# Performance work log

Measured on AMD Instinct MI355X. Metric: run time of the kernel, lower is better.

Reference implementation:

```python
import jax, jax.numpy as jnp
import numpy as np

B, T, D, U, P, E = 32, 10, 10, 50, 50, 256
EPS_ATTN = 1e-8
EPS_LN = 1e-5


def _layer_norm(x, w, b):
    mu = jnp.mean(x, axis=-1, keepdims=True)
    var = jnp.mean((x - mu) ** 2, axis=-1, keepdims=True)
    return (x - mu) / jnp.sqrt(var + EPS_LN) * w + b


def setup_inputs() -> dict:
    key = jax.random.key(0)
    ks = jax.random.split(key, 8)
    xavier = float(np.sqrt(2.0 / (E + E)))
    return {
        "Q": jax.random.normal(ks[0], (B, T, U, E), dtype=jnp.float32),
        "K": jax.random.normal(ks[1], (B, D, P, E), dtype=jnp.float32),
        "V": jax.random.normal(ks[2], (B, D, P, E), dtype=jnp.float32),
        "attention_mask": jnp.zeros((B, T, D, U, P), dtype=jnp.float32),
        "W1": jax.random.normal(ks[3], (E, E), dtype=jnp.float32) * xavier,
        "b1": jnp.zeros((E,), dtype=jnp.float32),
        "W2": jax.random.normal(ks[4], (E, E), dtype=jnp.float32) * xavier,
        "b2": jnp.zeros((E,), dtype=jnp.float32),
        "ln1_w": jnp.ones((E,), dtype=jnp.float32),
        "ln1_b": jnp.zeros((E,), dtype=jnp.float32),
        "ln2_w": jnp.ones((E,), dtype=jnp.float32),
        "ln2_b": jnp.zeros((E,), dtype=jnp.float32),
    }


def reference(Q, K, V, attention_mask, W1, b1, W2, b2, ln1_w, ln1_b, ln2_w, ln2_b):
    # dk = max(1.0, emb_dim); scale = sqrt(dk) + eps
    scale = jnp.sqrt(jnp.asarray(float(max(1.0, Q.shape[-1])), dtype=Q.dtype)) + EPS_ATTN
    # (B,T,D,U,P) attention logits
    qk = jnp.einsum("btue,bdpe->btdup", Q, K) / scale + attention_mask
    score = jax.nn.softmax(qk, axis=-1)
    v_att = jnp.einsum("btdup,bdpe->btdue", score, V)  # (B,T,D,U,E)
    x = Q[:, :, None, :, :] + v_att  # broadcast over doc dim
    x = _layer_norm(x, ln1_w, ln1_b)
    ffn = jnp.maximum(x @ W1.T + b1, 0.0) @ W2.T + b2
    return _layer_norm(ffn + x, ln2_w, ln2_b)
```

## Files before the change

kernel.cpp:

```cpp
#include <hip/hip_runtime.h>
#include <math.h>

#define Bsz 32
#define Tt  10
#define Dd  10
#define Uu  50
#define Pp  50
#define Ee  256

typedef __attribute__((ext_vector_type(8))) short bf16x8;
typedef __attribute__((ext_vector_type(4))) float f32x4;

#define STH 264
#define STV 72
#define STS 72

#define K1_OFF_V 0
#define K1_OFF_S 36864
#define K1_OFF_R 46080
#define K1_SMEM  47104

#define K3_OFF_X 0
#define K3_OFF_H 33792
#define K3_OFF_R 67584
#define K3_SMEM  69632
#define FFN_BM2 64

#define K2_OFF_H 0
#define K2_OFF_R 67584
#define K2_SMEM  71680
#define FFN_BM 128

#define WS_Q   0
#define WS_K   4096000
#define WS_V   8192000
#define WS_W1  12288000
#define WS_W2  12353536
#define WS_X   12419072
#define WS_NEED_BYTES 106758144ull

__device__ __forceinline__ unsigned short f2bf(float f) {
    unsigned u = __builtin_bit_cast(unsigned, f);
    u += 0x7fffu + ((u >> 16) & 1u);
    return (unsigned short)(u >> 16);
}
__device__ __forceinline__ float bf2f(unsigned short h) {
    unsigned u = ((unsigned)h) << 16;
    return __builtin_bit_cast(float, u);
}
__device__ __forceinline__ bf16x8 ldfrag(const unsigned short* p, int stride, int r0, int c0, int lane) {
    return *(const bf16x8*)(p + (size_t)(r0 + (lane & 15)) * stride + c0 + ((lane >> 4) << 3));
}
__device__ __forceinline__ bf16x8 bffrag(const unsigned short* __restrict__ base, int n, int k0, int lane) {
    const int row = n + (lane & 15);
    return *(const bf16x8*)(base + (size_t)row * 256 + k0 + ((lane >> 4) << 3));
}
__device__ __forceinline__ bf16x8 bffrag49(const unsigned short* __restrict__ base, int n, int k0, int lane) {
    int row = n + (lane & 15);
    row = row > 49 ? 49 : row;
    return *(const bf16x8*)(base + (size_t)row * 256 + k0 + ((lane >> 4) << 3));
}
__device__ __forceinline__ bf16x8 gfrag49(const float* __restrict__ base, int n, int k0, int lane) {
    int row = n + (lane & 15);
    row = row > 49 ? 49 : row;
    const int col = k0 + ((lane >> 4) << 3);
    const float4 a = *(const float4*)(base + (size_t)row * 256 + col);
    const float4 b = *(const float4*)(base + (size_t)row * 256 + col + 4);
    bf16x8 r;
    r[0] = (short)f2bf(a.x); r[1] = (short)f2bf(a.y); r[2] = (short)f2bf(a.z); r[3] = (short)f2bf(a.w);
    r[4] = (short)f2bf(b.x); r[5] = (short)f2bf(b.y); r[6] = (short)f2bf(b.z); r[7] = (short)f2bf(b.w);
    return r;
}
__device__ __forceinline__ bf16x8 xfrag(const float* __restrict__ base, int n, int k0, int lane) {
    const int row = n + (lane & 15);
    const int col = k0 + ((lane >> 4) << 3);
    const float4 a = *(const float4*)(base + (size_t)row * 256 + col);
    const float4 b = *(const float4*)(base + (size_t)row * 256 + col + 4);
    bf16x8 r;
    r[0] = (short)f2bf(a.x); r[1] = (short)f2bf(a.y); r[2] = (short)f2bf(a.z); r[3] = (short)f2bf(a.w);
    r[4] = (short)f2bf(b.x); r[5] = (short)f2bf(b.y); r[6] = (short)f2bf(b.z); r[7] = (short)f2bf(b.w);
    return r;
}
__device__ __forceinline__ bf16x8 wfrag(const unsigned short* wbf, const float* wf, int use_ws,
                                        int n, int k0, int lane) {
    const int row = n + (lane & 15);
    const int col = k0 + ((lane >> 4) << 3);
    if (use_ws) {
        return *(const bf16x8*)(wbf + (size_t)row * 256 + col);
    }
    const float4 a = *(const float4*)(wf + (size_t)row * 256 + col);
    const float4 b = *(const float4*)(wf + (size_t)row * 256 + col + 4);
    bf16x8 r;
    r[0] = (short)f2bf(a.x); r[1] = (short)f2bf(a.y); r[2] = (short)f2bf(a.z); r[3] = (short)f2bf(a.w);
    r[4] = (short)f2bf(b.x); r[5] = (short)f2bf(b.y); r[6] = (short)f2bf(b.z); r[7] = (short)f2bf(b.w);
    return r;
}

__global__ __launch_bounds__(256) void cvt_kernel(
    const float* __restrict__ Q, const float* __restrict__ K, const float* __restrict__ V,
    const float* __restrict__ W1, const float* __restrict__ W2, unsigned short* __restrict__ ws)
{
    const int blk = blockIdx.x, t = threadIdx.x;
    const float* src; unsigned short* dst; int f4base;
    if (blk < 1000)      { src = Q;  dst = ws + WS_Q;  f4base = blk * 1024; }
    else if (blk < 2000) { src = K;  dst = ws + WS_K;  f4base = (blk - 1000) * 1024; }
    else if (blk < 3000) { src = V;  dst = ws + WS_V;  f4base = (blk - 2000) * 1024; }
    else if (blk < 3016) { src = W1; dst = ws + WS_W1; f4base = (blk - 3000) * 1024; }
    else                 { src = W2; dst = ws + WS_W2; f4base = (blk - 3016) * 1024; }
    #pragma unroll
    for (int j = 0; j < 4; ++j) {
        int i4 = f4base + t + j * 256;
        float4 v = *(const float4*)(src + (size_t)i4 * 4);
        ushort4 o; o.x = f2bf(v.x); o.y = f2bf(v.y); o.z = f2bf(v.z); o.w = f2bf(v.w);
        *(ushort4*)(dst + (size_t)i4 * 4) = o;
    }
}

__global__ void convert_w_kernel(const float* __restrict__ W1, const float* __restrict__ W2,
                                 unsigned short* __restrict__ ws) {
    int i4 = (blockIdx.x * 256 + threadIdx.x) * 4;
    float4 a = *(const float4*)(W1 + i4);
    ushort4 oa; oa.x = f2bf(a.x); oa.y = f2bf(a.y); oa.z = f2bf(a.z); oa.w = f2bf(a.w);
    *(ushort4*)(ws + i4) = oa;
    float4 b = *(const float4*)(W2 + i4);
    ushort4 ob; ob.x = f2bf(b.x); ob.y = f2bf(b.y); ob.z = f2bf(b.z); ob.w = f2bf(b.w);
    *(ushort4*)(ws + 65536 + i4) = ob;
}

__global__ __launch_bounds__(512, 4) void attn_bf_kernel(
    const float* __restrict__ Q, const float* __restrict__ Msk,
    const float* __restrict__ ln1w, const float* __restrict__ ln1b,
    unsigned short* __restrict__ ws)
{
    __shared__ __align__(16) unsigned char smem[K1_SMEM];
    unsigned short* sVt = (unsigned short*)(smem + K1_OFF_V);
    unsigned short* sS  = (unsigned short*)(smem + K1_OFF_S);
    float*          red = (float*)(smem + K1_OFF_R);

    const int tid  = threadIdx.x;
    const int lane = tid & 63;
    const int wave = tid >> 6;
    const int quad = lane >> 4;
    const int l15  = lane & 15;

    const int btd = ((blockIdx.x & 7) * 400) + (blockIdx.x >> 3);
    const int b   = btd / (Tt * Dd);
    const int rem = btd % (Tt * Dd);
    const int t   = rem / Dd;
    const int d   = rem % Dd;

    const float* Qb = Q + ((size_t)(b * Tt + t) * Uu) * Ee;
    const unsigned short* Qbf = ws + WS_Q + (size_t)(b * Tt + t) * Uu * Ee;
    const unsigned short* Kbf = ws + WS_K + (size_t)(b * Dd + d) * Pp * Ee;
    const unsigned short* Vbf = ws + WS_V + (size_t)(b * Dd + d) * Pp * Ee;
    const float* Mb = Msk + ((size_t)((b * Tt + t) * Dd + d) * Uu) * Pp;
    unsigned short* Xbf = ws + WS_X + (size_t)btd * Uu * Ee;

    if (wave < 4) {
        const int mt = wave;
        int arow = mt * 16 + l15; if (arow > 49) arow = 49;
        const unsigned short* qrow = Qbf + (size_t)arow * Ee + (quad << 3);
        f32x4 acc[4];
        #pragma unroll
        for (int i = 0; i < 4; ++i) acc[i] = (f32x4){0.f, 0.f, 0.f, 0.f};
        #pragma unroll
        for (int k0 = 0; k0 < 256; k0 += 32) {
            bf16x8 a = *(const bf16x8*)(qrow + k0);
            #pragma unroll
            for (int nt = 0; nt < 4; ++nt) {
                bf16x8 bf = bffrag49(Kbf, nt << 4, k0, lane);
                acc[nt] = __builtin_amdgcn_mfma_f32_16x16x32_bf16(a, bf, acc[nt], 0, 0, 0);
            }
        }
        float l[4][4];
        #pragma unroll
        for (int nt = 0; nt < 4; ++nt) {
            int p = (nt << 4) + l15;
            #pragma unroll
            for (int r = 0; r < 4; ++r) {
                int u = mt * 16 + (quad << 2) + r;
                float v = acc[nt][r] * 0.0625f;
                if (p < Pp) { if (u < Uu) v += Mb[u * Pp + p]; }
                else v = -1e30f;
                l[nt][r] = v;
            }
        }
        #pragma unroll
        for (int r = 0; r < 4; ++r) {
            float m = fmaxf(fmaxf(l[0][r], l[1][r]), fmaxf(l[2][r], l[3][r]));
            #pragma unroll
            for (int msk = 1; msk < 16; msk <<= 1) m = fmaxf(m, __shfl_xor(m, msk));
            float e0 = __expf(l[0][r] - m), e1 = __expf(l[1][r] - m);
            float e2 = __expf(l[2][r] - m), e3 = __expf(l[3][r] - m);
            float s = e0 + e1 + e2 + e3;
            #pragma unroll
            for (int msk = 1; msk < 16; msk <<= 1) s += __shfl_xor(s, msk);
            float inv = 1.0f / s;
            int u = mt * 16 + (quad << 2) + r;
            sS[u * STS +  0 + l15] = f2bf(e0 * inv);
            sS[u * STS + 16 + l15] = f2bf(e1 * inv);
            sS[u * STS + 32 + l15] = f2bf(e2 * inv);
            sS[u * STS + 48 + l15] = f2bf(e3 * inv);
        }
    } else {
        const int lt = tid - 256;
        for (int i = lt; i < 1600; i += 256) {
            int p = i >> 5, e8 = (i & 31) << 3;
            bf16x8 v8 = *(const bf16x8*)(Vbf + (size_t)p * Ee + e8);
            #pragma unroll
            for (int j = 0; j < 8; ++j) sVt[(e8 + j) * STV + p] = (unsigned short)v8[j];
        }
        for (int i = lt; i < 3584; i += 256) {
            int p = 50 + (i >> 8), e = i & 255;
            sVt[e * STV + p] = 0;
        }
    }
    __syncthreads();

    {
        const int mt = wave >> 1;
        const int nh = (wave & 1) << 7;
        f32x4 acc[8];
        #pragma unroll
        for (int i = 0; i < 8; ++i) acc[i] = (f32x4){0.f, 0.f, 0.f, 0.f};
        #pragma unroll
        for (int k0 = 0; k0 < 64; k0 += 32) {
            bf16x8 a = ldfrag(sS, STS, mt << 4, k0, lane);
            #pragma unroll
            for (int nt = 0; nt < 8; ++nt) {
                bf16x8 bf = ldfrag(sVt, STV, nh + (nt << 4), k0, lane);
                acc[nt] = __builtin_amdgcn_mfma_f32_16x16x32_bf16(a, bf, acc[nt], 0, 0, 0);
            }
        }
        float s1[4] = {0.f, 0.f, 0.f, 0.f}, s2[4] = {0.f, 0.f, 0.f, 0.f};
        #pragma unroll
        for (int nt = 0; nt < 8; ++nt) {
            int e = nh + (nt << 4) + l15;
            #pragma unroll
            for (int r = 0; r < 4; ++r) {
                int u = (mt << 4) + (quad << 2) + r;
                float x = 0.f;
                if (u < Uu) x = acc[nt][r] + Qb[(size_t)u * Ee + e];
                acc[nt][r] = x;
                s1[r] += x; s2[r] += x * x;
            }
        }
        #pragma unroll
        for (int msk = 1; msk < 16; msk <<= 1) {
            #pragma unroll
            for (int r = 0; r < 4; ++r) { s1[r] += __shfl_xor(s1[r], msk); s2[r] += __shfl_xor(s2[r], msk); }
        }
        if (l15 == 0) {
            #pragma unroll
            for (int r = 0; r < 4; ++r) {
                int u = (mt << 4) + (quad << 2) + r;
                red[u * 4 + (wave & 1) * 2 + 0] = s1[r];
                red[u * 4 + (wave & 1) * 2 + 1] = s2[r];
            }
        }
        __syncthreads();
        #pragma unroll
        for (int r = 0; r < 4; ++r) {
            int u = (mt << 4) + (quad << 2) + r;
            if (u < Uu) {
                float sum = red[u * 4 + 0] + red[u * 4 + 2];
                float sq  = red[u * 4 + 1] + red[u * 4 + 3];
                float mu = sum * (1.0f / 256.0f);
                float var = sq * (1.0f / 256.0f) - mu * mu;
                float rstd = rsqrtf(var + 1e-5f);
                #pragma unroll
                for (int nt = 0; nt < 8; ++nt) {
                    int e = nh + (nt << 4) + l15;
                    Xbf[(size_t)u * Ee + e] = f2bf((acc[nt][r] - mu) * rstd * ln1w[e] + ln1b[e]);
                }
            }
        }
    }
}

__global__ __launch_bounds__(512, 4) void ffn_bf_kernel(
    const float* __restrict__ b1, const float* __restrict__ b2,
    const float* __restrict__ ln2w, const float* __restrict__ ln2b,
    const unsigned short* __restrict__ ws, float* __restrict__ out)
{
    __shared__ __align__(16) unsigned char smem[K3_SMEM];
    unsigned short* sX   = (unsigned short*)(smem + K3_OFF_X);
    unsigned short* sH   = (unsigned short*)(smem + K3_OFF_H);
    float*          red2 = (float*)(smem + K3_OFF_R);

    const int tid  = threadIdx.x;
    const int lane = tid & 63;
    const int wave = tid >> 6;
    const int quad = lane >> 4;
    const int l15  = lane & 15;

    const int mw = wave >> 2;
    const int nq = wave & 3;

    const size_t rowbase = (size_t)blockIdx.x * FFN_BM2;
    const unsigned short* Xbf  = ws + WS_X + rowbase * Ee;
    const unsigned short* W1bf = ws + WS_W1;
    const unsigned short* W2bf = ws + WS_W2;
    float* Ob = out + rowbase * Ee;

    {
        bf16x8 st[4];
        #pragma unroll
        for (int i = 0; i < 4; ++i) {
            int idx = tid + (i << 9);
            int r = idx >> 5, c8 = (idx & 31) << 3;
            st[i] = *(const bf16x8*)(Xbf + (size_t)r * Ee + c8);
        }
        #pragma unroll
        for (int i = 0; i < 4; ++i) {
            int idx = tid + (i << 9);
            int r = idx >> 5, c8 = (idx & 31) << 3;
            *(bf16x8*)(sX + r * STH + c8) = st[i];
        }
    }
    __syncthreads();

    {
        f32x4 acc[2][4];
        #pragma unroll
        for (int mi = 0; mi < 2; ++mi)
            #pragma unroll
            for (int nt = 0; nt < 4; ++nt) acc[mi][nt] = (f32x4){0.f, 0.f, 0.f, 0.f};
        float b1v[4];
        #pragma unroll
        for (int nt = 0; nt < 4; ++nt) b1v[nt] = b1[(nq << 6) + (nt << 4) + l15];
        #pragma unroll
        for (int k0 = 0; k0 < 256; k0 += 32) {
            bf16x8 a0 = ldfrag(sX, STH, (mw << 5),      k0, lane);
            bf16x8 a1 = ldfrag(sX, STH, (mw << 5) + 16, k0, lane);
            #pragma unroll
            for (int nt = 0; nt < 4; ++nt) {
                bf16x8 bf = bffrag(W1bf, (nq << 6) + (nt << 4), k0, lane);
                acc[0][nt] = __builtin_amdgcn_mfma_f32_16x16x32_bf16(a0, bf, acc[0][nt], 0, 0, 0);
                acc[1][nt] = __builtin_amdgcn_mfma_f32_16x16x32_bf16(a1, bf, acc[1][nt], 0, 0, 0);
            }
        }
        #pragma unroll
        for (int mi = 0; mi < 2; ++mi)
            #pragma unroll
            for (int nt = 0; nt < 4; ++nt) {
                int j = (nq << 6) + (nt << 4) + l15;
                #pragma unroll
                for (int r = 0; r < 4; ++r) {
                    int u = (mw << 5) + (mi << 4) + (quad << 2) + r;
                    sH[u * STH + j] = f2bf(fmaxf(acc[mi][nt][r] + b1v[nt], 0.f));
                }
            }
    }
    __syncthreads();

    {
        f32x4 acc[2][4];
        #pragma unroll
        for (int mi = 0; mi < 2; ++mi)
            #pragma unroll
            for (int nt = 0; nt < 4; ++nt) acc[mi][nt] = (f32x4){0.f, 0.f, 0.f, 0.f};
        float b2v[4], w2l[4], b2l[4];
        #pragma unroll
        for (int nt = 0; nt < 4; ++nt) {
            int j = (nq << 6) + (nt << 4) + l15;
            b2v[nt] = b2[j]; w2l[nt] = ln2w[j]; b2l[nt] = ln2b[j];
        }
        #pragma unroll
        for (int k0 = 0; k0 < 256; k0 += 32) {
            bf16x8 a0 = ldfrag(sH, STH, (mw << 5),      k0, lane);
            bf16x8 a1 = ldfrag(sH, STH, (mw << 5) + 16, k0, lane);
            #pragma unroll
            for (int nt = 0; nt < 4; ++nt) {
                bf16x8 bf = bffrag(W2bf, (nq << 6) + (nt << 4), k0, lane);
                acc[0][nt] = __builtin_amdgcn_mfma_f32_16x16x32_bf16(a0, bf, acc[0][nt], 0, 0, 0);
                acc[1][nt] = __builtin_amdgcn_mfma_f32_16x16x32_bf16(a1, bf, acc[1][nt], 0, 0, 0);
            }
        }
        #pragma unroll
        for (int mi = 0; mi < 2; ++mi) {
            float s1[4] = {0.f, 0.f, 0.f, 0.f}, s2[4] = {0.f, 0.f, 0.f, 0.f};
            #pragma unroll
            for (int nt = 0; nt < 4; ++nt) {
                int j = (nq << 6) + (nt << 4) + l15;
                #pragma unroll
                for (int r = 0; r < 4; ++r) {
                    int u = (mw << 5) + (mi << 4) + (quad << 2) + r;
                    float y = acc[mi][nt][r] + b2v[nt] + bf2f(sX[u * STH + j]);
                    acc[mi][nt][r] = y;
                    s1[r] += y; s2[r] += y * y;
                }
            }
            #pragma unroll
            for (int msk = 1; msk < 16; msk <<= 1)
                #pragma unroll
                for (int r = 0; r < 4; ++r) {
                    s1[r] += __shfl_xor(s1[r], msk);
                    s2[r] += __shfl_xor(s2[r], msk);
                }
            if (l15 == 0) {
                #pragma unroll
                for (int r = 0; r < 4; ++r) {
                    int u = (mw << 5) + (mi << 4) + (quad << 2) + r;
                    red2[u * 8 + nq * 2 + 0] = s1[r];
                    red2[u * 8 + nq * 2 + 1] = s2[r];
                }
            }
        }
        __syncthreads();
        #pragma unroll
        for (int mi = 0; mi < 2; ++mi)
            #pragma unroll
            for (int r = 0; r < 4; ++r) {
                int u = (mw << 5) + (mi << 4) + (quad << 2) + r;
                float sum = red2[u * 8 + 0] + red2[u * 8 + 2] + red2[u * 8 + 4] + red2[u * 8 + 6];
                float sq  = red2[u * 8 + 1] + red2[u * 8 + 3] + red2[u * 8 + 5] + red2[u * 8 + 7];
                float mu = sum * (1.0f / 256.0f);
                float var = sq * (1.0f / 256.0f) - mu * mu;
                float rstd = rsqrtf(var + 1e-5f);
                #pragma unroll
                for (int nt = 0; nt < 4; ++nt) {
                    int j = (nq << 6) + (nt << 4) + l15;
                    Ob[(size_t)u * Ee + j] = (acc[mi][nt][r] - mu) * rstd * w2l[nt] + b2l[nt];
                }
            }
    }
}

__global__ __launch_bounds__(512, 4) void attn_kernel(
    const float* __restrict__ Q,  const float* __restrict__ K,
    const float* __restrict__ V,  const float* __restrict__ Msk,
    const float* __restrict__ ln1w, const float* __restrict__ ln1b,
    float* __restrict__ out)
{
    __shared__ __align__(16) unsigned char smem[K1_SMEM];
    unsigned short* sVt = (unsigned short*)(smem + K1_OFF_V);
    unsigned short* sS  = (unsigned short*)(smem + K1_OFF_S);
    float*          red = (float*)(smem + K1_OFF_R);

    const int tid  = threadIdx.x;
    const int lane = tid & 63;
    const int wave = tid >> 6;
    const int quad = lane >> 4;
    const int l15  = lane & 15;

    const int btd = ((blockIdx.x & 7) * 400) + (blockIdx.x >> 3);
    const int b   = btd / (Tt * Dd);
    const int rem = btd % (Tt * Dd);
    const int t   = rem / Dd;
    const int d   = rem % Dd;

    const float* Qb = Q + ((size_t)(b * Tt + t) * Uu) * Ee;
    const float* Kb = K + ((size_t)(b * Dd + d) * Pp) * Ee;
    const float* Vb = V + ((size_t)(b * Dd + d) * Pp) * Ee;
    const float* Mb = Msk + ((size_t)((b * Tt + t) * Dd + d) * Uu) * Pp;
    float*       Xb = out + ((size_t)btd * Uu) * Ee;

    if (wave < 4) {
        const int mt = wave;
        int arow = mt * 16 + l15; if (arow > 49) arow = 49;
        const float* qrow = Qb + (size_t)arow * Ee + (quad << 3);
        f32x4 acc[4];
        #pragma unroll
        for (int i = 0; i < 4; ++i) acc[i] = (f32x4){0.f, 0.f, 0.f, 0.f};
        #pragma unroll
        for (int k0 = 0; k0 < 256; k0 += 32) {
            float4 qa = *(const float4*)(qrow + k0);
            float4 qb = *(const float4*)(qrow + k0 + 4);
            bf16x8 a;
            a[0] = (short)f2bf(qa.x); a[1] = (short)f2bf(qa.y); a[2] = (short)f2bf(qa.z); a[3] = (short)f2bf(qa.w);
            a[4] = (short)f2bf(qb.x); a[5] = (short)f2bf(qb.y); a[6] = (short)f2bf(qb.z); a[7] = (short)f2bf(qb.w);
            #pragma unroll
            for (int nt = 0; nt < 4; ++nt) {
                bf16x8 bf = gfrag49(Kb, nt << 4, k0, lane);
                acc[nt] = __builtin_amdgcn_mfma_f32_16x16x32_bf16(a, bf, acc[nt], 0, 0, 0);
            }
        }
        float l[4][4];
        #pragma unroll
        for (int nt = 0; nt < 4; ++nt) {
            int p = (nt << 4) + l15;
            #pragma unroll
            for (int r = 0; r < 4; ++r) {
                int u = mt * 16 + (quad << 2) + r;
                float v = acc[nt][r] * 0.0625f;
                if (p < Pp) { if (u < Uu) v += Mb[u * Pp + p]; }
                else v = -1e30f;
                l[nt][r] = v;
            }
        }
        #pragma unroll
        for (int r = 0; r < 4; ++r) {
            float m = fmaxf(fmaxf(l[0][r], l[1][r]), fmaxf(l[2][r], l[3][r]));
            #pragma unroll
            for (int msk = 1; msk < 16; msk <<= 1) m = fmaxf(m, __shfl_xor(m, msk));
            float e0 = __expf(l[0][r] - m), e1 = __expf(l[1][r] - m);
            float e2 = __expf(l[2][r] - m), e3 = __expf(l[3][r] - m);
            float s = e0 + e1 + e2 + e3;
            #pragma unroll
            for (int msk = 1; msk < 16; msk <<= 1) s += __shfl_xor(s, msk);
            float inv = 1.0f / s;
            int u = mt * 16 + (quad << 2) + r;
            sS[u * STS +  0 + l15] = f2bf(e0 * inv);
            sS[u * STS + 16 + l15] = f2bf(e1 * inv);
            sS[u * STS + 32 + l15] = f2bf(e2 * inv);
            sS[u * STS + 48 + l15] = f2bf(e3 * inv);
        }
    } else {
        const int lt = tid - 256;
        #pragma unroll 4
        for (int i = lt; i < 12800; i += 256) {
            int p = i >> 8, e = i & 255;
            sVt[e * STV + p] = f2bf(Vb[p * Ee + e]);
        }
        for (int i = lt; i < 3584; i += 256) {
            int p = 50 + (i >> 8), e = i & 255;
            sVt[e * STV + p] = 0;
        }
    }
    __syncthreads();

    {
        const int mt = wave >> 1;
        const int nh = (wave & 1) << 7;
        f32x4 acc[8];
        #pragma unroll
        for (int i = 0; i < 8; ++i) acc[i] = (f32x4){0.f, 0.f, 0.f, 0.f};
        #pragma unroll
        for (int k0 = 0; k0 < 64; k0 += 32) {
            bf16x8 a = ldfrag(sS, STS, mt << 4, k0, lane);
            #pragma unroll
            for (int nt = 0; nt < 8; ++nt) {
                bf16x8 bf = ldfrag(sVt, STV, nh + (nt << 4), k0, lane);
                acc[nt] = __builtin_amdgcn_mfma_f32_16x16x32_bf16(a, bf, acc[nt], 0, 0, 0);
            }
        }
        float s1[4] = {0.f, 0.f, 0.f, 0.f}, s2[4] = {0.f, 0.f, 0.f, 0.f};
        #pragma unroll
        for (int nt = 0; nt < 8; ++nt) {
            int e = nh + (nt << 4) + l15;
            #pragma unroll
            for (int r = 0; r < 4; ++r) {
                int u = (mt << 4) + (quad << 2) + r;
                float x = 0.f;
                if (u < Uu) x = acc[nt][r] + Qb[(size_t)u * Ee + e];
                acc[nt][r] = x;
                s1[r] += x; s2[r] += x * x;
            }
        }
        #pragma unroll
        for (int msk = 1; msk < 16; msk <<= 1) {
            #pragma unroll
            for (int r = 0; r < 4; ++r) { s1[r] += __shfl_xor(s1[r], msk); s2[r] += __shfl_xor(s2[r], msk); }
        }
        if (l15 == 0) {
            #pragma unroll
            for (int r = 0; r < 4; ++r) {
                int u = (mt << 4) + (quad << 2) + r;
                red[u * 4 + (wave & 1) * 2 + 0] = s1[r];
                red[u * 4 + (wave & 1) * 2 + 1] = s2[r];
            }
        }
        __syncthreads();
        #pragma unroll
        for (int r = 0; r < 4; ++r) {
            int u = (mt << 4) + (quad << 2) + r;
            if (u < Uu) {
                float sum = red[u * 4 + 0] + red[u * 4 + 2];
                float sq  = red[u * 4 + 1] + red[u * 4 + 3];
                float mu = sum * (1.0f / 256.0f);
                float var = sq * (1.0f / 256.0f) - mu * mu;
                float rstd = rsqrtf(var + 1e-5f);
                #pragma unroll
                for (int nt = 0; nt < 8; ++nt) {
                    int e = nh + (nt << 4) + l15;
                    Xb[(size_t)u * Ee + e] = (acc[nt][r] - mu) * rstd * ln1w[e] + ln1b[e];
                }
            }
        }
    }
}

__global__ __launch_bounds__(512, 4) void ffn_kernel(
    const float* __restrict__ W1, const float* __restrict__ b1,
    const float* __restrict__ W2, const float* __restrict__ b2,
    const float* __restrict__ ln2w, const float* __restrict__ ln2b,
    const unsigned short* __restrict__ wsbf, int use_ws,
    float* __restrict__ out)
{
    __shared__ __align__(16) unsigned char smem[K2_SMEM];
    unsigned short* sH   = (unsigned short*)(smem + K2_OFF_H);
    float*          red2 = (float*)(smem + K2_OFF_R);

    const int tid  = threadIdx.x;
    const int lane = tid & 63;
    const int wave = tid >> 6;
    const int quad = lane >> 4;
    const int l15  = lane & 15;

    const int mw = wave >> 2;
    const int nq = wave & 3;

    const size_t rowbase = (size_t)blockIdx.x * FFN_BM;
    const float* Xb = out + rowbase * Ee;
    float*       Ob = out + rowbase * Ee;

    {
        f32x4 acc[4][4];
        #pragma unroll
        for (int mi = 0; mi < 4; ++mi)
            #pragma unroll
            for (int nt = 0; nt < 4; ++nt) acc[mi][nt] = (f32x4){0.f, 0.f, 0.f, 0.f};
        float b1v[4];
        #pragma unroll
        for (int nt = 0; nt < 4; ++nt) b1v[nt] = b1[(nq << 6) + (nt << 4) + l15];
        #pragma unroll
        for (int k0 = 0; k0 < 256; k0 += 32) {
            bf16x8 a[4];
            #pragma unroll
            for (int mi = 0; mi < 4; ++mi) a[mi] = xfrag(Xb, (mw << 6) + (mi << 4), k0, lane);
            #pragma unroll
            for (int nt = 0; nt < 4; ++nt) {
                bf16x8 bf = wfrag(wsbf, W1, use_ws, (nq << 6) + (nt << 4), k0, lane);
                #pragma unroll
                for (int mi = 0; mi < 4; ++mi)
                    acc[mi][nt] = __builtin_amdgcn_mfma_f32_16x16x32_bf16(a[mi], bf, acc[mi][nt], 0, 0, 0);
            }
        }
        #pragma unroll
        for (int mi = 0; mi < 4; ++mi)
            #pragma unroll
            for (int nt = 0; nt < 4; ++nt) {
                int j = (nq << 6) + (nt << 4) + l15;
                #pragma unroll
                for (int r = 0; r < 4; ++r) {
                    int u = (mw << 6) + (mi << 4) + (quad << 2) + r;
                    sH[u * STH + j] = f2bf(fmaxf(acc[mi][nt][r] + b1v[nt], 0.f));
                }
            }
    }
    __syncthreads();

    {
        f32x4 acc[4][4];
        #pragma unroll
        for (int mi = 0; mi < 4; ++mi)
            #pragma unroll
            for (int nt = 0; nt < 4; ++nt) acc[mi][nt] = (f32x4){0.f, 0.f, 0.f, 0.f};
        float b2v[4], w2l[4], b2l[4];
        #pragma unroll
        for (int nt = 0; nt < 4; ++nt) {
            int j = (nq << 6) + (nt << 4) + l15;
            b2v[nt] = b2[j]; w2l[nt] = ln2w[j]; b2l[nt] = ln2b[j];
        }
        #pragma unroll
        for (int k0 = 0; k0 < 256; k0 += 32) {
            bf16x8 a[4];
            #pragma unroll
            for (int mi = 0; mi < 4; ++mi) a[mi] = ldfrag(sH, STH, (mw << 6) + (mi << 4), k0, lane);
            #pragma unroll
            for (int nt = 0; nt < 4; ++nt) {
                bf16x8 bf = wfrag(wsbf + 65536, W2, use_ws, (nq << 6) + (nt << 4), k0, lane);
                #pragma unroll
                for (int mi = 0; mi < 4; ++mi)
                    acc[mi][nt] = __builtin_amdgcn_mfma_f32_16x16x32_bf16(a[mi], bf, acc[mi][nt], 0, 0, 0);
            }
        }
        #pragma unroll
        for (int mi = 0; mi < 4; ++mi) {
            float s1[4] = {0.f, 0.f, 0.f, 0.f}, s2[4] = {0.f, 0.f, 0.f, 0.f};
            #pragma unroll
            for (int nt = 0; nt < 4; ++nt) {
                int j = (nq << 6) + (nt << 4) + l15;
                #pragma unroll
                for (int r = 0; r < 4; ++r) {
                    int u = (mw << 6) + (mi << 4) + (quad << 2) + r;
                    float y = acc[mi][nt][r] + b2v[nt] + Xb[(size_t)u * Ee + j];
                    acc[mi][nt][r] = y;
                    s1[r] += y; s2[r] += y * y;
                }
            }
            #pragma unroll
            for (int msk = 1; msk < 16; msk <<= 1)
                #pragma unroll
                for (int r = 0; r < 4; ++r) {
                    s1[r] += __shfl_xor(s1[r], msk);
                    s2[r] += __shfl_xor(s2[r], msk);
                }
            if (l15 == 0) {
                #pragma unroll
                for (int r = 0; r < 4; ++r) {
                    int u = (mw << 6) + (mi << 4) + (quad << 2) + r;
                    red2[u * 8 + nq * 2 + 0] = s1[r];
                    red2[u * 8 + nq * 2 + 1] = s2[r];
                }
            }
        }
        __syncthreads();
        #pragma unroll
        for (int mi = 0; mi < 4; ++mi)
            #pragma unroll
            for (int r = 0; r < 4; ++r) {
                int u = (mw << 6) + (mi << 4) + (quad << 2) + r;
                float sum = red2[u * 8 + 0] + red2[u * 8 + 2] + red2[u * 8 + 4] + red2[u * 8 + 6];
                float sq  = red2[u * 8 + 1] + red2[u * 8 + 3] + red2[u * 8 + 5] + red2[u * 8 + 7];
                float mu = sum * (1.0f / 256.0f);
                float var = sq * (1.0f / 256.0f) - mu * mu;
                float rstd = rsqrtf(var + 1e-5f);
                #pragma unroll
                for (int nt = 0; nt < 4; ++nt) {
                    int j = (nq << 6) + (nt << 4) + l15;
                    Ob[(size_t)u * Ee + j] = (acc[mi][nt][r] - mu) * rstd * w2l[nt] + b2l[nt];
                }
            }
    }
}

extern "C" void kernel_launch(void* const* d_in, const int* in_sizes, int n_in,
                              void* d_out, int out_size, void* d_ws, size_t ws_size,
                              hipStream_t stream) {
    const float* Q    = (const float*)d_in[0];
    const float* K    = (const float*)d_in[1];
    const float* V    = (const float*)d_in[2];
    const float* M    = (const float*)d_in[3];
    const float* W1   = (const float*)d_in[4];
    const float* b1   = (const float*)d_in[5];
    const float* W2   = (const float*)d_in[6];
    const float* b2   = (const float*)d_in[7];
    const float* ln1w = (const float*)d_in[8];
    const float* ln1b = (const float*)d_in[9];
    const float* ln2w = (const float*)d_in[10];
    const float* ln2b = (const float*)d_in[11];
    float* out = (float*)d_out;

    if (ws_size >= WS_NEED_BYTES) {
        unsigned short* ws = (unsigned short*)d_ws;
        cvt_kernel<<<3032, 256, 0, stream>>>(Q, K, V, W1, W2, ws);
        attn_bf_kernel<<<Bsz * Tt * Dd, 512, 0, stream>>>(Q, M, ln1w, ln1b, ws);
        ffn_bf_kernel<<<(Bsz * Tt * Dd * Uu) / FFN_BM2, 512, 0, stream>>>(b1, b2, ln2w, ln2b,
                                                                          ws, out);
    } else {
        int use_ws = (ws_size >= 262144) ? 1 : 0;
        const unsigned short* wsbf = (const unsigned short*)d_ws;
        if (use_ws) {
            convert_w_kernel<<<64, 256, 0, stream>>>(W1, W2, (unsigned short*)d_ws);
        }
        attn_kernel<<<Bsz * Tt * Dd, 512, 0, stream>>>(Q, K, V, M, ln1w, ln1b, out);
        ffn_kernel<<<(Bsz * Tt * Dd * Uu) / FFN_BM, 512, 0, stream>>>(W1, b1, W2, b2, ln2w, ln2b,
                                                                      wsbf, use_ws, out);
    }
}
```

Before: 541.0 us.

## Read FFN X tile directly from global and rotate V transpose stores

The FFN kernel no longer stages the 64-row X tile in LDS. It loads A fragments and the residual values straight from global memory, which roughly halves LDS use and drops one barrier, so more blocks can be resident per CU. In exchange every wave re-reads X from global/L2 and the residual reads are scattered scalar loads. Separately, the V-transpose loop in the attention kernel rotates its store order per lane to spread LDS bank conflicts.

New measurement: 576.6 us. 6.6% more time.

```diff
diff --git a/kernel.cpp b/kernel.cpp
--- a/kernel.cpp
+++ b/kernel.cpp
@@ -20,10 +20,9 @@
 #define K1_OFF_R 46080
 #define K1_SMEM  47104
 
-#define K3_OFF_X 0
-#define K3_OFF_H 33792
-#define K3_OFF_R 67584
-#define K3_SMEM  69632
+#define K4_OFF_H 0
+#define K4_OFF_R 33792
+#define K4_SMEM  35840
 #define FFN_BM2 64
 
 #define K2_OFF_H 0
@@ -204,11 +203,15 @@
         }
     } else {
         const int lt = tid - 256;
+        const int rot = lt & 7;
         for (int i = lt; i < 1600; i += 256) {
             int p = i >> 5, e8 = (i & 31) << 3;
             bf16x8 v8 = *(const bf16x8*)(Vbf + (size_t)p * Ee + e8);
             #pragma unroll
-            for (int j = 0; j < 8; ++j) sVt[(e8 + j) * STV + p] = (unsigned short)v8[j];
+            for (int m = 0; m < 8; ++m) {
+                int j = (m + rot) & 7;
+                sVt[(e8 + j) * STV + p] = (unsigned short)v8[j];
+            }
         }
         for (int i = lt; i < 3584; i += 256) {
             int p = 50 + (i >> 8), e = i & 255;
@@ -283,10 +286,9 @@
     const float* __restrict__ ln2w, const float* __restrict__ ln2b,
     const unsigned short* __restrict__ ws, float* __restrict__ out)
 {
-    __shared__ __align__(16) unsigned char smem[K3_SMEM];
-    unsigned short* sX   = (unsigned short*)(smem + K3_OFF_X);
-    unsigned short* sH   = (unsigned short*)(smem + K3_OFF_H);
-    float*          red2 = (float*)(smem + K3_OFF_R);
+    __shared__ __align__(16) unsigned char smem[K4_SMEM];
+    unsigned short* sH   = (unsigned short*)(smem + K4_OFF_H);
+    float*          red2 = (float*)(smem + K4_OFF_R);
 
     const int tid  = threadIdx.x;
     const int lane = tid & 63;
@@ -304,23 +306,6 @@
     float* Ob = out + rowbase * Ee;
 
     {
-        bf16x8 st[4];
-        #pragma unroll
-        for (int i = 0; i < 4; ++i) {
-            int idx = tid + (i << 9);
-            int r = idx >> 5, c8 = (idx & 31) << 3;
-            st[i] = *(const bf16x8*)(Xbf + (size_t)r * Ee + c8);
-        }
-        #pragma unroll
-        for (int i = 0; i < 4; ++i) {
-            int idx = tid + (i << 9);
-            int r = idx >> 5, c8 = (idx & 31) << 3;
-            *(bf16x8*)(sX + r * STH + c8) = st[i];
-        }
-    }
-    __syncthreads();
-
-    {
         f32x4 acc[2][4];
         #pragma unroll
         for (int mi = 0; mi < 2; ++mi)
@@ -331,8 +316,8 @@
         for (int nt = 0; nt < 4; ++nt) b1v[nt] = b1[(nq << 6) + (nt << 4) + l15];
         #pragma unroll
         for (int k0 = 0; k0 < 256; k0 += 32) {
-            bf16x8 a0 = ldfrag(sX, STH, (mw << 5),      k0, lane);
-            bf16x8 a1 = ldfrag(sX, STH, (mw << 5) + 16, k0, lane);
+            bf16x8 a0 = bffrag(Xbf, (mw << 5),      k0, lane);
+            bf16x8 a1 = bffrag(Xbf, (mw << 5) + 16, k0, lane);
             #pragma unroll
             for (int nt = 0; nt < 4; ++nt) {
                 bf16x8 bf = bffrag(W1bf, (nq << 6) + (nt << 4), k0, lane);
@@ -386,7 +371,7 @@
                 #pragma unroll
                 for (int r = 0; r < 4; ++r) {
                     int u = (mw << 5) + (mi << 4) + (quad << 2) + r;
-                    float y = acc[mi][nt][r] + b2v[nt] + bf2f(sX[u * STH + j]);
+                    float y = acc[mi][nt][r] + b2v[nt] + bf2f(Xbf[(size_t)u * Ee + j]);
                     acc[mi][nt][r] = y;
                     s1[r] += y; s2[r] += y * y;
                 }
```
